# Kernel optimization log

Measured on AMD Instinct MI355X. Metric: run time of the kernel, lower is better.

Reference implementation:

```python
import jax, jax.numpy as jnp
import numpy as np

EPS = 1e-5

def _bn(x):
    # training-mode batchnorm (batch stats), gamma=1 beta=0 per the module's init
    ax = tuple(range(x.ndim - 1))
    m = x.mean(ax, keepdims=True)
    v = x.var(ax, keepdims=True)
    return (x - m) * jax.lax.rsqrt(v + EPS)

def _mlp(x, weights):
    # shared 1x1-conv MLP: pointwise linear -> BN -> ReLU
    for W in weights:
        x = jax.nn.relu(_bn(jnp.einsum('...c,oc->...o', x, W)))
    return x

def _fps_single(xyz, npoint):
    # farthest point sampling, xyz [N,3] -> [npoint] int32 indices
    N = xyz.shape[0]
    def step(carry, _):
        dists, far = carry
        d = jnp.sum((xyz - xyz[far]) ** 2, -1)
        dists = jnp.minimum(dists, d)
        return (dists, jnp.argmax(dists).astype(jnp.int32)), far
    init = (jnp.full((N,), 1e10, xyz.dtype), jnp.int32(0))
    _, idx = jax.lax.scan(step, init, None, length=npoint)
    return idx

def _ball_query(new_xyz, xyz, radius, nsample):
    # first nsample points (in original order) within radius of each center
    d2 = jnp.sum((new_xyz[:, :, None, :] - xyz[:, None, :, :]) ** 2, -1)  # [B,S,N]
    N = xyz.shape[1]
    rank = jnp.where(d2 < radius * radius, jnp.arange(N, dtype=jnp.int32), jnp.int32(N))
    vals, _ = jax.lax.top_k(-rank, nsample)
    idx = -vals
    idx = jnp.where(idx == N, idx[..., :1], idx)  # pad with first valid (center itself)
    return idx

def _gather(pts, idx):
    # pts [B,N,C], idx [B,S,ns] -> [B,S,ns,C]
    B, S, ns = idx.shape
    return jnp.take_along_axis(pts, idx.reshape(B, S * ns, 1), axis=1).reshape(B, S, ns, pts.shape[-1])

def _sa(xyz, feats, npoint, radius, nsample, weights):
    fps_idx = jax.vmap(_fps_single, in_axes=(0, None))(xyz, npoint)
    new_xyz = jnp.take_along_axis(xyz, fps_idx[:, :, None], axis=1)  # [B,S,3]
    idx = _ball_query(new_xyz, xyz, radius, nsample)
    g_xyz = (_gather(xyz, idx) - new_xyz[:, :, None, :]) / radius  # normalize_xyz
    x = g_xyz if feats is None else jnp.concatenate([g_xyz, _gather(feats, idx)], -1)
    x = _mlp(x, weights)
    return new_xyz, x.max(axis=2), fps_idx  # maxpool over nsample

def _forward(obj_cloud, gripper_cloud, sa1_w0, sa1_w1, sa1_w2, sa2_w0, sa2_w1, sa2_w2,
             sa3_w0, sa3_w1, sa3_w2, ge_w0, ge_w1, ge_w2,
             head_w0, head_b0, head_w1, head_b1, head_w2, head_b2):
    # gripper encoder: pointwise conv1d MLP + global maxpool
    g = _mlp(gripper_cloud, [ge_w0, ge_w1, ge_w2])      # [B,G,128]
    gripper_feature = g.max(axis=1)                      # [B,128]
    # backbone
    xyz1, f1, _ = _sa(obj_cloud, None, 512, 0.2, 32, [sa1_w0, sa1_w1, sa1_w2])
    xyz2, f2, _ = _sa(xyz1, f1, 128, 0.4, 64, [sa2_w0, sa2_w1, sa2_w2])
    # sa3: group_all (use_xyz, no centering/normalization)
    x = jnp.concatenate([xyz2, f2], -1)[:, None]         # [B,1,128,259]
    x = _mlp(x, [sa3_w0, sa3_w1, sa3_w2])
    obj_feature = x.max(axis=2)[:, 0]                    # [B,1024]
    comb = jnp.concatenate([gripper_feature, obj_feature], -1)  # [B,1152]
    h = _bn(comb)
    h = jax.nn.relu(_bn(h @ head_w0.T + head_b0))
    h = jax.nn.relu(_bn(h @ head_w1.T + head_b1))
    return jax.nn.relu(h @ head_w2.T + head_b2)          # [B,1]

def setup_inputs() -> dict:
    key = jax.random.key(0)
    ks = jax.random.split(key, 24)
    def w(k, o, i):
        return (jax.random.normal(k, (o, i), jnp.float32) * 0.05)
    inp = {
        'obj_cloud': jax.random.uniform(ks[0], (8, 20000, 3), jnp.float32),
        'gripper_cloud': jax.random.uniform(ks[1], (8, 512, 3), jnp.float32),
        'sa1_w0': w(ks[2], 64, 3),   'sa1_w1': w(ks[3], 64, 64),   'sa1_w2': w(ks[4], 128, 64),
        'sa2_w0': w(ks[5], 128, 131),'sa2_w1': w(ks[6], 128, 128), 'sa2_w2': w(ks[7], 256, 128),
        'sa3_w0': w(ks[8], 256, 259),'sa3_w1': w(ks[9], 512, 256), 'sa3_w2': w(ks[10], 1024, 512),
        'ge_w0': w(ks[11], 64, 3),   'ge_w1': w(ks[12], 128, 64),  'ge_w2': w(ks[13], 128, 128),
        'head_w0': w(ks[14], 512, 1152), 'head_b0': jnp.zeros((512,), jnp.float32),
        'head_w1': w(ks[15], 256, 512),  'head_b1': jnp.zeros((256,), jnp.float32),
        'head_w2': w(ks[16], 1, 256),    'head_b2': jnp.zeros((1,), jnp.float32),
    }
    return inp

def reference(obj_cloud, gripper_cloud, sa1_w0, sa1_w1, sa1_w2, sa2_w0, sa2_w1, sa2_w2,
              sa3_w0, sa3_w1, sa3_w2, ge_w0, ge_w1, ge_w2,
              head_w0, head_b0, head_w1, head_b1, head_w2, head_b2):
    return _forward(obj_cloud, gripper_cloud, sa1_w0, sa1_w1, sa1_w2, sa2_w0, sa2_w1, sa2_w2,
                    sa3_w0, sa3_w1, sa3_w2, ge_w0, ge_w1, ge_w2,
                    head_w0, head_b0, head_w1, head_b1, head_w2, head_b2)
```

## Files before the change

### kernel.cpp

```cpp
#include <hip/hip_runtime.h>
#include <cstddef>
#include <cstdint>

#define EPS_BN 1e-5f
#define NBINS 4
#define NEG_INF (-__builtin_inff())

template <bool FUSE_IN>
__global__ __launch_bounds__(256) void gemm_xwt(const float* __restrict__ X,
                                                const float* __restrict__ Wm,
                                                float* __restrict__ Y,
                                                int R, int Cin, int Cout,
                                                const float* __restrict__ st_in, int Rin,
                                                float* __restrict__ st_out) {
  __shared__ __align__(16) float Xs[16][132];
  __shared__ __align__(16) float Ws[16][132];
  __shared__ float sMean[512], sScale[512];
  const int t  = threadIdx.x;
  const int r0 = blockIdx.x << 7;
  const int n0 = blockIdx.y << 7;
  const int tx = t & 15;
  const int ty = t >> 4;

  if constexpr (FUSE_IN) {
    const float inv = 1.f / (float)Rin;
    for (int k = t; k < Cin; k += 256) {
      float s = 0.f, q = 0.f;
#pragma unroll
      for (int bn = 0; bn < NBINS; ++bn) {
        s += st_in[bn * 2 * Cin + k];
        q += st_in[bn * 2 * Cin + Cin + k];
      }
      const float m  = s * inv;
      const float vr = fmaf(-m, m, q * inv);
      sMean[k]  = m;
      sScale[k] = rsqrtf(vr + EPS_BN);
    }
    __syncthreads();
  }

  float acc[8][8] = {};
  const int rStage = t >> 1;
  const int kBase  = (t & 1) << 3;
  const int nr     = n0 + rStage;

  for (int k0 = 0; k0 < Cin; k0 += 16) {
    const float* xrow = X  + (size_t)(r0 + rStage) * Cin + k0 + kBase;
    const float* wrow = Wm + (size_t)nr * Cin + k0 + kBase;
    if (((Cin & 3) == 0) && (k0 + 16 <= Cin)) {
      float4 xa = *(const float4*)(xrow);
      float4 xb = *(const float4*)(xrow + 4);
      if constexpr (FUSE_IN) {
        const int kb = k0 + kBase;
        xa.x = fmaxf(0.f, (xa.x - sMean[kb + 0]) * sScale[kb + 0]);
        xa.y = fmaxf(0.f, (xa.y - sMean[kb + 1]) * sScale[kb + 1]);
        xa.z = fmaxf(0.f, (xa.z - sMean[kb + 2]) * sScale[kb + 2]);
        xa.w = fmaxf(0.f, (xa.w - sMean[kb + 3]) * sScale[kb + 3]);
        xb.x = fmaxf(0.f, (xb.x - sMean[kb + 4]) * sScale[kb + 4]);
        xb.y = fmaxf(0.f, (xb.y - sMean[kb + 5]) * sScale[kb + 5]);
        xb.z = fmaxf(0.f, (xb.z - sMean[kb + 6]) * sScale[kb + 6]);
        xb.w = fmaxf(0.f, (xb.w - sMean[kb + 7]) * sScale[kb + 7]);
      }
      Xs[kBase + 0][rStage] = xa.x; Xs[kBase + 1][rStage] = xa.y;
      Xs[kBase + 2][rStage] = xa.z; Xs[kBase + 3][rStage] = xa.w;
      Xs[kBase + 4][rStage] = xb.x; Xs[kBase + 5][rStage] = xb.y;
      Xs[kBase + 6][rStage] = xb.z; Xs[kBase + 7][rStage] = xb.w;
      float4 wa = {0, 0, 0, 0}, wb = {0, 0, 0, 0};
      if (nr < Cout) { wa = *(const float4*)(wrow); wb = *(const float4*)(wrow + 4); }
      Ws[kBase + 0][rStage] = wa.x; Ws[kBase + 1][rStage] = wa.y;
      Ws[kBase + 2][rStage] = wa.z; Ws[kBase + 3][rStage] = wa.w;
      Ws[kBase + 4][rStage] = wb.x; Ws[kBase + 5][rStage] = wb.y;
      Ws[kBase + 6][rStage] = wb.z; Ws[kBase + 7][rStage] = wb.w;
    } else {
#pragma unroll
      for (int u = 0; u < 8; ++u) {
        const int k = k0 + kBase + u;
        float xe = 0.f, we = 0.f;
        if (k < Cin) {
          xe = xrow[u];
          if constexpr (FUSE_IN) xe = fmaxf(0.f, (xe - sMean[k]) * sScale[k]);
          if (nr < Cout) we = wrow[u];
        }
        Xs[kBase + u][rStage] = xe;
        Ws[kBase + u][rStage] = we;
      }
    }
    __syncthreads();
#pragma unroll
    for (int kk = 0; kk < 16; ++kk) {
      const float4 a0 = *(const float4*)(&Xs[kk][ty << 2]);
      const float4 a1 = *(const float4*)(&Xs[kk][64 + (ty << 2)]);
      const float4 b0 = *(const float4*)(&Ws[kk][tx << 2]);
      const float4 b1 = *(const float4*)(&Ws[kk][64 + (tx << 2)]);
      const float av[8] = {a0.x, a0.y, a0.z, a0.w, a1.x, a1.y, a1.z, a1.w};
      const float bw[8] = {b0.x, b0.y, b0.z, b0.w, b1.x, b1.y, b1.z, b1.w};
#pragma unroll
      for (int i = 0; i < 8; ++i)
#pragma unroll
        for (int j = 0; j < 8; ++j) acc[i][j] = fmaf(av[i], bw[j], acc[i][j]);
    }
    __syncthreads();
  }
#pragma unroll
  for (int h = 0; h < 2; ++h)
#pragma unroll
    for (int i = 0; i < 4; ++i) {
      const int r = r0 + h * 64 + (ty << 2) + i;
      float* yr = Y + (size_t)r * Cout;
#pragma unroll
      for (int g = 0; g < 2; ++g) {
        const int n = n0 + g * 64 + (tx << 2);
        if (n < Cout) {
          float4 o = {acc[h * 4 + i][g * 4 + 0], acc[h * 4 + i][g * 4 + 1],
                      acc[h * 4 + i][g * 4 + 2], acc[h * 4 + i][g * 4 + 3]};
          *(float4*)(yr + n) = o;
        }
      }
    }
#pragma unroll
  for (int g = 0; g < 2; ++g)
#pragma unroll
    for (int j = 0; j < 4; ++j) {
      float s = 0.f, q = 0.f;
#pragma unroll
      for (int rh = 0; rh < 8; ++rh) {
        const float v = acc[rh][g * 4 + j];
        s += v;
        q = fmaf(v, v, q);
      }
      Xs[ty][g * 64 + (tx << 2) + j] = s;
      Ws[ty][g * 64 + (tx << 2) + j] = q;
    }
  __syncthreads();
  if (t < 128) {
    const int n = n0 + t;
    if (n < Cout) {
      float s = 0.f, q = 0.f;
#pragma unroll
      for (int w = 0; w < 16; ++w) { s += Xs[w][t]; q += Ws[w][t]; }
      float* dst = st_out + (blockIdx.x & (NBINS - 1)) * 2 * Cout;
      atomicAdd(dst + n, s);
      atomicAdd(dst + Cout + n, q);
    }
  }
}

__global__ void bn_apply_relu_maxpool(const float* __restrict__ Y,
                                      const float* __restrict__ st,
                                      float* __restrict__ o, int G, int ns, int C) {
  const int i = blockIdx.x * 256 + threadIdx.x;
  if (i >= G * C) return;
  const int c = i % C;
  const int g = i / C;
  float s = 0.f, q = 0.f;
#pragma unroll
  for (int bn = 0; bn < NBINS; ++bn) {
    s += st[bn * 2 * C + c];
    q += st[bn * 2 * C + C + c];
  }
  const int R = G * ns;
  const float inv = 1.f / (float)R;
  const float m  = s * inv;
  const float vr = fmaf(-m, m, q * inv);
  const float sc = rsqrtf(vr + EPS_BN);
  const float* p = Y + (size_t)g * ns * C + c;
  float mx = NEG_INF;
  for (int k = 0; k < ns; ++k) mx = fmaxf(mx, p[(size_t)k * C]);
  o[i] = fmaxf(0.f, (mx - m) * sc);
}

#define REPA(X) X(0) X(1) X(2) X(3) X(4) X(5) X(6) X(7) X(8) X(9) X(10) X(11)
#define REPB(X) X(12) X(13) X(14) X(15) X(16) X(17) X(18) X(19)

__global__ __launch_bounds__(1024)
void fps_sa1_kernel(const float* __restrict__ xyz, float* __restrict__ new_xyz) {
  const int b    = blockIdx.x;
  const int tid  = threadIdx.x;
  const int lane = tid & 63;
  const int wave = tid >> 6;
  const float* p = xyz + (size_t)b * 20000 * 3;

  __shared__ float ddL[12 * 1024];
  __shared__ float sv[16], sx[16], sy[16], sz[16];
  __shared__ int   si[16];
  __shared__ float bc[3];

#define DECLR(k) float px##k, py##k, pz##k, dd##k;
  REPB(DECLR)
#undef DECLR

#define INITL(k) ddL[(k) * 1024 + tid] = 1e10f;
  REPA(INITL)
#undef INITL
#define INITR(k) {                                                          \
    const int i = tid + (k) * 1024;                                         \
    if (i < 20000) {                                                        \
      px##k = p[i * 3 + 0]; py##k = p[i * 3 + 1]; pz##k = p[i * 3 + 2];     \
      dd##k = 1e10f;                                                        \
    } else {                                                                \
      px##k = 0.f; py##k = 0.f; pz##k = 0.f;                                \
      dd##k = NEG_INF;                                                      \
    } }
  REPB(INITR)
#undef INITR

  float fx = p[0], fy = p[1], fz = p[2];
  if (tid == 0) {
    float* o = new_xyz + (size_t)b * 512 * 3;
    o[0] = fx; o[1] = fy; o[2] = fz;
  }
  __syncthreads();

  for (int s = 1; s < 512; ++s) {
    float bv = NEG_INF;
    int   bi = 0x7fffffff;
    float bx = 0.f, by = 0.f, bz = 0.f;
#define SCANS(k) {                                                          \
    const int i = tid + (k) * 1024;                                         \
    const float qx = p[i * 3 + 0], qy = p[i * 3 + 1], qz = p[i * 3 + 2];    \
    const float dx = qx - fx, dy = qy - fy, dz = qz - fz;                   \
    const float d  = __fadd_rn(__fadd_rn(__fmul_rn(dx, dx), __fmul_rn(dy, dy)), \
                               __fmul_rn(dz, dz));                          \
    const float nd = fminf(ddL[(k) * 1024 + tid], d);                       \
    ddL[(k) * 1024 + tid] = nd;                                             \
    if (nd > bv) { bv = nd; bi = i; bx = qx; by = qy; bz = qz; } }
    REPA(SCANS)
#undef SCANS
#define SCANR(k) {                                                          \
    const float dx = px##k - fx, dy = py##k - fy, dz = pz##k - fz;          \
    const float d  = __fadd_rn(__fadd_rn(__fmul_rn(dx, dx), __fmul_rn(dy, dy)), \
                               __fmul_rn(dz, dz));                          \
    const float nd = fminf(dd##k, d);                                       \
    dd##k = nd;                                                             \
    if (nd > bv) { bv = nd; bi = tid + (k) * 1024;                          \
                   bx = px##k; by = py##k; bz = pz##k; } }
    REPB(SCANR)
#undef SCANR
    float v  = bv;
    int   i0 = bi;
#pragma unroll
    for (int m = 1; m < 64; m <<= 1) {
      const float ov = __shfl_xor(v, m, 64);
      const int   oi = __shfl_xor(i0, m, 64);
      if (ov > v || (ov == v && oi < i0)) { v = ov; i0 = oi; }
    }
    if (i0 == bi) {
      sv[wave] = bv; si[wave] = bi; sx[wave] = bx; sy[wave] = by; sz[wave] = bz;
    }
    __syncthreads();
    if (tid < 64) {
      const float lv = (lane < 16) ? sv[lane] : NEG_INF;
      const int   li = (lane < 16) ? si[lane] : 0x7fffffff;
      float v2 = lv;
      int   i2 = li;
#pragma unroll
      for (int m = 1; m < 16; m <<= 1) {
        const float ov = __shfl_xor(v2, m, 64);
        const int   oi = __shfl_xor(i2, m, 64);
        if (ov > v2 || (ov == v2 && oi < i2)) { v2 = ov; i2 = oi; }
      }
      if (lane < 16 && li == i2) {
        const float wx = sx[lane], wy = sy[lane], wz = sz[lane];
        bc[0] = wx; bc[1] = wy; bc[2] = wz;
        float* o = new_xyz + ((size_t)b * 512 + s) * 3;
        o[0] = wx; o[1] = wy; o[2] = wz;
      }
    }
    __syncthreads();
    fx = bc[0]; fy = bc[1]; fz = bc[2];
  }
}

template <int N, int NP, int THREADS, int NPT>
__global__ __launch_bounds__(THREADS)
void fps2_kernel(const float* __restrict__ xyz, float* __restrict__ new_xyz) {
  constexpr int NW = THREADS / 64;
  const int b    = blockIdx.x;
  const int tid  = threadIdx.x;
  const int lane = tid & 63;
  const int wave = tid >> 6;
  const float* p = xyz + (size_t)b * N * 3;
  float px[NPT], py[NPT], pz[NPT], dd[NPT];
#pragma unroll
  for (int j = 0; j < NPT; ++j) {
    const int i = tid + j * THREADS;
    if (i < N) {
      px[j] = p[i * 3 + 0];
      py[j] = p[i * 3 + 1];
      pz[j] = p[i * 3 + 2];
      dd[j] = 1e10f;
    } else {
      px[j] = 0.f; py[j] = 0.f; pz[j] = 0.f;
      dd[j] = NEG_INF;
    }
  }
  __shared__ float sv[NW], sx[NW], sy[NW], sz[NW];
  __shared__ int   si[NW];
  __shared__ float bc[3];
  float fx = p[0], fy = p[1], fz = p[2];
  if (tid == 0) {
    float* o = new_xyz + (size_t)b * NP * 3;
    o[0] = fx; o[1] = fy; o[2] = fz;
  }
  for (int s = 1; s < NP; ++s) {
    float bv = NEG_INF;
    int   bi = 0x7fffffff;
    float bx = 0.f, by = 0.f, bz = 0.f;
#pragma unroll
    for (int j = 0; j < NPT; ++j) {
      const float dx = px[j] - fx;
      const float dy = py[j] - fy;
      const float dz = pz[j] - fz;
      const float d  = __fadd_rn(__fadd_rn(__fmul_rn(dx, dx), __fmul_rn(dy, dy)),
                                 __fmul_rn(dz, dz));
      const float nd = fminf(dd[j], d);
      dd[j] = nd;
      if (nd > bv) { bv = nd; bi = tid + j * THREADS; bx = px[j]; by = py[j]; bz = pz[j]; }
    }
    float v = bv;
    int   i0 = bi;
#pragma unroll
    for (int m = 1; m < 64; m <<= 1) {
      const float ov = __shfl_xor(v, m, 64);
      const int   oi = __shfl_xor(i0, m, 64);
      if (ov > v || (ov == v && oi < i0)) { v = ov; i0 = oi; }
    }
    if (i0 == bi) {
      sv[wave] = bv; si[wave] = bi; sx[wave] = bx; sy[wave] = by; sz[wave] = bz;
    }
    __syncthreads();
    if (tid < 64) {
      const float lv = (lane < NW) ? sv[lane] : NEG_INF;
      const int   li = (lane < NW) ? si[lane] : 0x7fffffff;
      float v2 = lv;
      int   i2 = li;
#pragma unroll
      for (int m = 1; m < NW; m <<= 1) {
        const float ov = __shfl_xor(v2, m, 64);
        const int   oi = __shfl_xor(i2, m, 64);
        if (ov > v2 || (ov == v2 && oi < i2)) { v2 = ov; i2 = oi; }
      }
      if (lane < NW && li == i2) {
        const float wx = sx[lane], wy = sy[lane], wz = sz[lane];
        bc[0] = wx; bc[1] = wy; bc[2] = wz;
        float* o = new_xyz + ((size_t)b * NP + s) * 3;
        o[0] = wx; o[1] = wy; o[2] = wz;
      }
    }
    __syncthreads();
    fx = bc[0]; fy = bc[1]; fz = bc[2];
  }
}

template <int N, int NS>
__global__ __launch_bounds__(256)
void ballquery_wave_kernel(const float* __restrict__ centers,
                           const float* __restrict__ pts,
                           int* __restrict__ idx, int BS, int S, float r2) {
  const int w    = (blockIdx.x * 256 + threadIdx.x) >> 6;
  const int lane = threadIdx.x & 63;
  if (w >= BS) return;
  const int b = w / S;
  const float cx = centers[w * 3 + 0];
  const float cy = centers[w * 3 + 1];
  const float cz = centers[w * 3 + 2];
  const float* p = pts + (size_t)b * N * 3;
  int* o = idx + (size_t)w * NS;
  int total = 0;
  int first = -1;
  for (int i0 = 0; i0 < N && total < NS; i0 += 64) {
    const int i = i0 + lane;
    bool pred = false;
    if (i < N) {
      const float dx = cx - p[i * 3 + 0];
      const float dy = cy - p[i * 3 + 1];
      const float dz = cz - p[i * 3 + 2];
      const float d2 = __fadd_rn(__fadd_rn(__fmul_rn(dx, dx), __fmul_rn(dy, dy)),
                                 __fmul_rn(dz, dz));
      pred = (d2 < r2);
    }
    const unsigned long long mask = __ballot(pred);
    if (mask) {
      const unsigned long long below = (lane == 0) ? 0ull : (mask << (64 - lane));
      const int before = __popcll(below);
      if (pred && (total + before) < NS) o[total + before] = i;
      if (first < 0) first = i0 + (__ffsll((long long)mask) - 1);
      total += __popcll(mask);
    }
  }
  if (lane >= total && lane < NS) o[lane] = first;
}

__global__ void group1_kernel(const float* __restrict__ xyz, const float* __restrict__ ctr,
                              const int* __restrict__ idx, float* __restrict__ X1) {
  const int t = blockIdx.x * 256 + threadIdx.x;
  if (t >= 8 * 512 * 32) return;
  const int g = t >> 5;
  const int b = g >> 9;
  const int i = idx[t];
  const float* p = xyz + ((size_t)b * 20000 + i) * 3;
  const float* c = ctr + (size_t)g * 3;
  X1[t * 3 + 0] = (p[0] - c[0]) / 0.2f;
  X1[t * 3 + 1] = (p[1] - c[1]) / 0.2f;
  X1[t * 3 + 2] = (p[2] - c[2]) / 0.2f;
}

__global__ void group2_kernel(const float* __restrict__ xyz1,
                              const float* __restrict__ xyz2,
                              const float* __restrict__ f1,
                              const int* __restrict__ idx2,
                              float* __restrict__ X2) {
  const int t = blockIdx.x * 256 + threadIdx.x;
  if (t >= 65536 * 131) return;
  const int r = t / 131;
  const int c = t - r * 131;
  const int g = r >> 6;
  const int b = g >> 7;
  const int i = idx2[r];
  float v;
  if (c < 3) {
    v = (xyz1[((size_t)b * 512 + i) * 3 + c] - xyz2[(size_t)g * 3 + c]) / 0.4f;
  } else {
    v = f1[((size_t)b * 512 + i) * 128 + (c - 3)];
  }
  X2[t] = v;
}

__global__ void build_x3_kernel(const float* __restrict__ xyz2, const float* __restrict__ f2,
                                float* __restrict__ X3) {
  const int t = blockIdx.x * 256 + threadIdx.x;
  if (t >= 1024 * 259) return;
  const int r = t / 259;
  const int c = t - r * 259;
  X3[t] = (c < 3) ? xyz2[r * 3 + c] : f2[(size_t)r * 256 + (c - 3)];
}

__global__ __launch_bounds__(512) void head_kernel(
    const float* __restrict__ gfeat, const float* __restrict__ objf,
    const float* __restrict__ w0, const float* __restrict__ b0,
    const float* __restrict__ w1, const float* __restrict__ b1,
    const float* __restrict__ w2, const float* __restrict__ b2,
    float* __restrict__ out) {
  __shared__ __align__(16) float comb[8 * 1152];
  __shared__ __align__(16) float h1[8 * 512];
  __shared__ __align__(16) float h2[8 * 256];
  const int tid = threadIdx.x;
  for (int i = tid; i < 8 * 1152; i += 512) {
    const int b = i / 1152, c = i - b * 1152;
    comb[i] = (c < 128) ? gfeat[b * 128 + c] : objf[b * 1024 + (c - 128)];
  }
  __syncthreads();
  for (int c = tid; c < 1152; c += 512) {
    float s = 0.f;
#pragma unroll
    for (int b = 0; b < 8; ++b) s += comb[b * 1152 + c];
    const float m = s * 0.125f;
    float v = 0.f;
#pragma unroll
    for (int b = 0; b < 8; ++b) { const float d = comb[b * 1152 + c] - m; v = fmaf(d, d, v); }
    const float sc = rsqrtf(v * 0.125f + EPS_BN);
#pragma unroll
    for (int b = 0; b < 8; ++b) comb[b * 1152 + c] = (comb[b * 1152 + c] - m) * sc;
  }
  __syncthreads();
  {
    float a[8];
#pragma unroll
    for (int b = 0; b < 8; ++b) a[b] = b0[tid];
    const float* wr = w0 + (size_t)tid * 1152;
    for (int ci = 0; ci < 1152; ci += 4) {
      const float4 wv = *(const float4*)(wr + ci);
#pragma unroll
      for (int b = 0; b < 8; ++b) {
        const float4 xv = *(const float4*)(&comb[b * 1152 + ci]);
        a[b] = fmaf(xv.x, wv.x, a[b]);
        a[b] = fmaf(xv.y, wv.y, a[b]);
        a[b] = fmaf(xv.z, wv.z, a[b]);
        a[b] = fmaf(xv.w, wv.w, a[b]);
      }
    }
    float s = 0.f;
#pragma unroll
    for (int b = 0; b < 8; ++b) s += a[b];
    const float m = s * 0.125f;
    float v = 0.f;
#pragma unroll
    for (int b = 0; b < 8; ++b) { const float d = a[b] - m; v = fmaf(d, d, v); }
    const float sc = rsqrtf(v * 0.125f + EPS_BN);
#pragma unroll
    for (int b = 0; b < 8; ++b) h1[b * 512 + tid] = fmaxf(0.f, (a[b] - m) * sc);
  }
  __syncthreads();
  if (tid < 256) {
    float a[8];
#pragma unroll
    for (int b = 0; b < 8; ++b) a[b] = b1[tid];
    const float* wr = w1 + (size_t)tid * 512;
    for (int ci = 0; ci < 512; ci += 4) {
      const float4 wv = *(const float4*)(wr + ci);
#pragma unroll
      for (int b = 0; b < 8; ++b) {
        const float4 xv = *(const float4*)(&h1[b * 512 + ci]);
        a[b] = fmaf(xv.x, wv.x, a[b]);
        a[b] = fmaf(xv.y, wv.y, a[b]);
        a[b] = fmaf(xv.z, wv.z, a[b]);
        a[b] = fmaf(xv.w, wv.w, a[b]);
      }
    }
    float s = 0.f;
#pragma unroll
    for (int b = 0; b < 8; ++b) s += a[b];
    const float m = s * 0.125f;
    float v = 0.f;
#pragma unroll
    for (int b = 0; b < 8; ++b) { const float d = a[b] - m; v = fmaf(d, d, v); }
    const float sc = rsqrtf(v * 0.125f + EPS_BN);
#pragma unroll
    for (int b = 0; b < 8; ++b) h2[b * 256 + tid] = fmaxf(0.f, (a[b] - m) * sc);
  }
  __syncthreads();
  if (tid < 8) {
    float s = b2[0];
    for (int ci = 0; ci < 256; ++ci) s = fmaf(h2[tid * 256 + ci], w2[ci], s);
    out[tid] = fmaxf(0.f, s);
  }
}

extern "C" void kernel_launch(void* const* d_in, const int* in_sizes, int n_in,
                              void* d_out, int out_size, void* d_ws, size_t ws_size,
                              hipStream_t stream) {
  (void)in_sizes; (void)n_in; (void)out_size; (void)ws_size;
  const float* obj  = (const float*)d_in[0];
  const float* grip = (const float*)d_in[1];
  const float* s1w0 = (const float*)d_in[2];
  const float* s1w1 = (const float*)d_in[3];
  const float* s1w2 = (const float*)d_in[4];
  const float* s2w0 = (const float*)d_in[5];
  const float* s2w1 = (const float*)d_in[6];
  const float* s2w2 = (const float*)d_in[7];
  const float* s3w0 = (const float*)d_in[8];
  const float* s3w1 = (const float*)d_in[9];
  const float* s3w2 = (const float*)d_in[10];
  const float* gw0  = (const float*)d_in[11];
  const float* gw1  = (const float*)d_in[12];
  const float* gw2  = (const float*)d_in[13];
  const float* hw0  = (const float*)d_in[14];
  const float* hb0  = (const float*)d_in[15];
  const float* hw1  = (const float*)d_in[16];
  const float* hb1  = (const float*)d_in[17];
  const float* hw2  = (const float*)d_in[18];
  const float* hb2  = (const float*)d_in[19];
  float* out = (float*)d_out;

  float* wsf   = (float*)d_ws;
  float* stats = wsf;
  float* xyz1  = wsf + 23040;
  float* xyz2  = wsf + 35328;
  float* gfeat = wsf + 38400;
  float* objf  = wsf + 39424;
  float* f1    = wsf + 47616;
  float* f2    = wsf + 571904;
  float* x3    = wsf + 834048;
  int*   idx1  = (int*)(wsf + 1099264);
  int*   idx2  = (int*)(wsf + 1230336);
  float* bufP  = wsf + 1295872;
  float* bufQ  = wsf + 18073088;

  static const int st_off[12] = {0, 512, 1536, 2560, 3072, 3584,
                                 4608, 5632, 6656, 8704, 10752, 14848};
  auto st = [&](int li) { return stats + st_off[li]; };

  hipMemsetAsync(stats, 0, 23040 * sizeof(float), stream);

  auto gemm0 = [&](const float* X, const float* Wm, float* Y, int R, int Cin, int Cout,
                   int lo) {
    dim3 g((R + 127) / 128, (Cout + 127) / 128);
    gemm_xwt<false><<<g, 256, 0, stream>>>(X, Wm, Y, R, Cin, Cout, nullptr, 0, st(lo));
  };
  auto gemmf = [&](const float* X, const float* Wm, float* Y, int R, int Cin, int Cout,
                   int li, int lo) {
    dim3 g((R + 127) / 128, (Cout + 127) / 128);
    gemm_xwt<true><<<g, 256, 0, stream>>>(X, Wm, Y, R, Cin, Cout, st(li), R, st(lo));
  };
  auto applymax_k = [&](const float* Y, int li, int G, int ns, int C, float* o) {
    const int n = G * C;
    bn_apply_relu_maxpool<<<(n + 255) / 256, 256, 0, stream>>>(Y, st(li), o, G, ns, C);
  };

  fps_sa1_kernel<<<8, 1024, 0, stream>>>(obj, xyz1);

  float* gY1 = bufP;
  float* gY2 = bufP + 262144;
  float* gY3 = bufP + 786432;
  gemm0(grip, gw0, gY1, 4096, 3, 64, 0);
  gemmf(gY1, gw1, gY2, 4096, 64, 128, 0, 1);
  gemmf(gY2, gw2, gY3, 4096, 128, 128, 1, 2);
  applymax_k(gY3, 2, 8, 512, 128, gfeat);

  ballquery_wave_kernel<20000, 32><<<1024, 256, 0, stream>>>(xyz1, obj, idx1, 4096, 512, 0.04f);
  float* X1 = bufQ;
  group1_kernel<<<512, 256, 0, stream>>>(obj, xyz1, idx1, X1);
  gemm0(X1, s1w0, bufP, 131072, 3, 64, 3);
  gemmf(bufP, s1w1, bufQ, 131072, 64, 64, 3, 4);
  gemmf(bufQ, s1w2, bufP, 131072, 64, 128, 4, 5);
  applymax_k(bufP, 5, 4096, 32, 128, f1);

  fps2_kernel<512, 128, 256, 2><<<8, 256, 0, stream>>>(xyz1, xyz2);
  ballquery_wave_kernel<512, 64><<<256, 256, 0, stream>>>(xyz2, xyz1, idx2, 1024, 128, 0.16f);
  float* X2 = bufQ;
  group2_kernel<<<(65536 * 131 + 255) / 256, 256, 0, stream>>>(xyz1, xyz2, f1, idx2, X2);
  gemm0(X2, s2w0, bufP, 65536, 131, 128, 6);
  gemmf(bufP, s2w1, bufQ, 65536, 128, 128, 6, 7);
  gemmf(bufQ, s2w2, bufP, 65536, 128, 256, 7, 8);
  applymax_k(bufP, 8, 1024, 64, 256, f2);

  build_x3_kernel<<<(1024 * 259 + 255) / 256, 256, 0, stream>>>(xyz2, f2, x3);
  float* Y3a = bufQ;
  float* Y3b = bufQ + 262144;
  float* Y3c = bufQ + 786432;
  gemm0(x3, s3w0, Y3a, 1024, 259, 256, 9);
  gemmf(Y3a, s3w1, Y3b, 1024, 256, 512, 9, 10);
  gemmf(Y3b, s3w2, Y3c, 1024, 512, 1024, 10, 11);
  applymax_k(Y3c, 11, 8, 128, 1024, objf);

  head_kernel<<<1, 512, 0, stream>>>(gfeat, objf, hw0, hb0, hw1, hb1, hw2, hb2, out);
}
```

Before: 2.489 ms.

## Sort FPS points by Morton cell and skip threads via bounding-box pruning

Adds a pre-pass that bins each cloud's 20000 points into a 16^3 Morton grid and writes them spatially sorted as float4 (xyz plus original index) into a scratch buffer. The FPS kernel then gives each thread 20 contiguous sorted points with a per-thread bounding box. When the new far point is farther from the box than the thread's current best distance, the thread skips its distance update entirely. This cuts the per-iteration distance work across 511 serial steps, at the cost of an extra sort kernel and a larger LDS distance array. Ties are broken by the original index so results stay identical.

Measured after the change: 3.016 ms. 21.2% more time.

```diff
diff --git a/kernel.cpp b/kernel.cpp
--- a/kernel.cpp
+++ b/kernel.cpp
@@ -169,40 +169,95 @@
   o[i] = fmaxf(0.f, (mx - m) * sc);
 }
 
-#define REPA(X) X(0) X(1) X(2) X(3) X(4) X(5) X(6) X(7) X(8) X(9) X(10) X(11)
-#define REPB(X) X(12) X(13) X(14) X(15) X(16) X(17) X(18) X(19)
+__device__ inline int fps_cell(float x, float y, float z) {
+  int cx = (int)(x * 16.f); cx = cx < 0 ? 0 : (cx > 15 ? 15 : cx);
+  int cy = (int)(y * 16.f); cy = cy < 0 ? 0 : (cy > 15 ? 15 : cy);
+  int cz = (int)(z * 16.f); cz = cz < 0 ? 0 : (cz > 15 ? 15 : cz);
+  auto sp = [](int v) { return (v & 1) | ((v & 2) << 2) | ((v & 4) << 4) | ((v & 8) << 6); };
+  return sp(cx) | (sp(cy) << 1) | (sp(cz) << 2);
+}
 
 __global__ __launch_bounds__(1024)
-void fps_sa1_kernel(const float* __restrict__ xyz, float* __restrict__ new_xyz) {
+void fps_sort_kernel(const float* __restrict__ xyz, float4* __restrict__ sorted) {
+  const int b = blockIdx.x, tid = threadIdx.x;
+  const float* p = xyz + (size_t)b * 20000 * 3;
+  __shared__ int hist[4096];
+  __shared__ int base[4096];
+  __shared__ int wsum[64];
+  for (int i = tid; i < 4096; i += 1024) hist[i] = 0;
+  __syncthreads();
+#pragma unroll
+  for (int k = 0; k < 20; ++k) {
+    const int i = tid + k * 1024;
+    if (i < 20000) atomicAdd(&hist[fps_cell(p[i * 3], p[i * 3 + 1], p[i * 3 + 2])], 1);
+  }
+  __syncthreads();
+  if (tid < 64) {
+    int s = 0;
+    for (int j = 0; j < 64; ++j) s += hist[tid * 64 + j];
+    wsum[tid] = s;
+  }
+  __syncthreads();
+  if (tid == 0) {
+    int r = 0;
+    for (int j = 0; j < 64; ++j) { const int v = wsum[j]; wsum[j] = r; r += v; }
+  }
+  __syncthreads();
+  if (tid < 64) {
+    int r = wsum[tid];
+    for (int j = 0; j < 64; ++j) { const int c = tid * 64 + j; const int h = hist[c]; base[c] = r; r += h; }
+  }
+  __syncthreads();
+  float4* sb = sorted + (size_t)b * 20480;
+#pragma unroll
+  for (int k = 0; k < 20; ++k) {
+    const int i = tid + k * 1024;
+    if (i < 20000) {
+      const float x = p[i * 3], y = p[i * 3 + 1], z = p[i * 3 + 2];
+      const int pos = atomicAdd(&base[fps_cell(x, y, z)], 1);
+      float4 q; q.x = x; q.y = y; q.z = z; q.w = __int_as_float(i);
+      sb[pos] = q;
+    }
+  }
+  const float x0 = p[0], y0 = p[1], z0 = p[2];
+  for (int i = 20000 + tid; i < 20480; i += 1024) {
+    float4 q; q.x = x0; q.y = y0; q.z = z0; q.w = __int_as_float(0x3fffffff);
+    sb[i] = q;
+  }
+}
+
+__global__ __launch_bounds__(1024)
+void fps_sa1_kernel(const float* __restrict__ xyz, const float4* __restrict__ sorted,
+                    float* __restrict__ new_xyz) {
   const int b    = blockIdx.x;
   const int tid  = threadIdx.x;
   const int lane = tid & 63;
   const int wave = tid >> 6;
   const float* p = xyz + (size_t)b * 20000 * 3;
-
-  __shared__ float ddL[12 * 1024];
+  const float4* sp = sorted + (size_t)b * 20480 + tid * 20;
+
+  __shared__ float ddL[20 * 1024];
   __shared__ float sv[16], sx[16], sy[16], sz[16];
   __shared__ int   si[16];
   __shared__ float bc[3];
 
-#define DECLR(k) float px##k, py##k, pz##k, dd##k;
-  REPB(DECLR)
-#undef DECLR
-
-#define INITL(k) ddL[(k) * 1024 + tid] = 1e10f;
-  REPA(INITL)
-#undef INITL
-#define INITR(k) {                                                          \
-    const int i = tid + (k) * 1024;                                         \
-    if (i < 20000) {                                                        \
-      px##k = p[i * 3 + 0]; py##k = p[i * 3 + 1]; pz##k = p[i * 3 + 2];     \
-      dd##k = 1e10f;                                                        \
-    } else {                                                                \
-      px##k = 0.f; py##k = 0.f; pz##k = 0.f;                                \
-      dd##k = NEG_INF;                                                      \
-    } }
-  REPB(INITR)
-#undef INITR
+  float mnx = 1e30f, mny = 1e30f, mnz = 1e30f;
+  float mxx = -1e30f, mxy = -1e30f, mxz = -1e30f;
+  float cbv = NEG_INF, cbx = 0.f, cby = 0.f, cbz = 0.f;
+  int   cbi = 0x7fffffff;
+
+#pragma unroll
+  for (int j = 0; j < 20; ++j) {
+    const float4 q = sp[j];
+    const int qi = __float_as_int(q.w);
+    mnx = fminf(mnx, q.x); mny = fminf(mny, q.y); mnz = fminf(mnz, q.z);
+    mxx = fmaxf(mxx, q.x); mxy = fmaxf(mxy, q.y); mxz = fmaxf(mxz, q.z);
+    const float d0 = (qi < 20000) ? 1e10f : NEG_INF;
+    ddL[j * 1024 + tid] = d0;
+    if (d0 > cbv || (d0 == cbv && qi < cbi)) {
+      cbv = d0; cbi = qi; cbx = q.x; cby = q.y; cbz = q.z;
+    }
+  }
 
   float fx = p[0], fy = p[1], fz = p[2];
   if (tid == 0) {
@@ -212,40 +267,38 @@
   __syncthreads();
 
   for (int s = 1; s < 512; ++s) {
-    float bv = NEG_INF;
-    int   bi = 0x7fffffff;
-    float bx = 0.f, by = 0.f, bz = 0.f;
-#define SCANS(k) {                                                          \
-    const int i = tid + (k) * 1024;                                         \
-    const float qx = p[i * 3 + 0], qy = p[i * 3 + 1], qz = p[i * 3 + 2];    \
-    const float dx = qx - fx, dy = qy - fy, dz = qz - fz;                   \
-    const float d  = __fadd_rn(__fadd_rn(__fmul_rn(dx, dx), __fmul_rn(dy, dy)), \
-                               __fmul_rn(dz, dz));                          \
-    const float nd = fminf(ddL[(k) * 1024 + tid], d);                       \
-    ddL[(k) * 1024 + tid] = nd;                                             \
-    if (nd > bv) { bv = nd; bi = i; bx = qx; by = qy; bz = qz; } }
-    REPA(SCANS)
-#undef SCANS
-#define SCANR(k) {                                                          \
-    const float dx = px##k - fx, dy = py##k - fy, dz = pz##k - fz;          \
-    const float d  = __fadd_rn(__fadd_rn(__fmul_rn(dx, dx), __fmul_rn(dy, dy)), \
-                               __fmul_rn(dz, dz));                          \
-    const float nd = fminf(dd##k, d);                                       \
-    dd##k = nd;                                                             \
-    if (nd > bv) { bv = nd; bi = tid + (k) * 1024;                          \
-                   bx = px##k; by = py##k; bz = pz##k; } }
-    REPB(SCANR)
-#undef SCANR
-    float v  = bv;
-    int   i0 = bi;
+    const float ax = fmaxf(fmaxf(mnx - fx, fx - mxx), 0.f);
+    const float ay = fmaxf(fmaxf(mny - fy, fy - mxy), 0.f);
+    const float az = fmaxf(fmaxf(mnz - fz, fz - mxz), 0.f);
+    const float dm = __fadd_rn(__fadd_rn(__fmul_rn(ax, ax), __fmul_rn(ay, ay)),
+                               __fmul_rn(az, az));
+    if (dm < cbv) {
+      cbv = NEG_INF; cbi = 0x7fffffff;
+#pragma unroll
+      for (int j = 0; j < 20; ++j) {
+        const float4 q = sp[j];
+        const int qi = __float_as_int(q.w);
+        const float dx = q.x - fx, dy = q.y - fy, dz = q.z - fz;
+        const float d = __fadd_rn(__fadd_rn(__fmul_rn(dx, dx), __fmul_rn(dy, dy)),
+                                  __fmul_rn(dz, dz));
+        const int a = j * 1024 + tid;
+        const float nd = fminf(ddL[a], d);
+        ddL[a] = nd;
+        if (nd > cbv || (nd == cbv && qi < cbi)) {
+          cbv = nd; cbi = qi; cbx = q.x; cby = q.y; cbz = q.z;
+        }
+      }
+    }
+    float v  = cbv;
+    int   i0 = cbi;
 #pragma unroll
     for (int m = 1; m < 64; m <<= 1) {
       const float ov = __shfl_xor(v, m, 64);
       const int   oi = __shfl_xor(i0, m, 64);
       if (ov > v || (ov == v && oi < i0)) { v = ov; i0 = oi; }
     }
-    if (i0 == bi) {
-      sv[wave] = bv; si[wave] = bi; sx[wave] = bx; sy[wave] = by; sz[wave] = bz;
+    if (i0 == cbi) {
+      sv[wave] = cbv; si[wave] = cbi; sx[wave] = cbx; sy[wave] = cby; sz[wave] = cbz;
     }
     __syncthreads();
     if (tid < 64) {
@@ -587,7 +640,9 @@
     bn_apply_relu_maxpool<<<(n + 255) / 256, 256, 0, stream>>>(Y, st(li), o, G, ns, C);
   };
 
-  fps_sa1_kernel<<<8, 1024, 0, stream>>>(obj, xyz1);
+  float4* sorted = (float4*)bufP;
+  fps_sort_kernel<<<8, 1024, 0, stream>>>(obj, sorted);
+  fps_sa1_kernel<<<8, 1024, 0, stream>>>(obj, sorted, xyz1);
 
   float* gY1 = bufP;
   float* gY2 = bufP + 262144;
```

## Restructure SA1 FPS: contiguous per-thread points, float4 loads, single-barrier reduction

Applied to the files above, without the earlier changes.

Each thread in the SA1 farthest-point-sampling kernel now owns 20 contiguous points instead of strided ones. The 12 spilled points are read with float4 vector loads, and threads at or above 1000 are padded with -inf distances. The cross-wave argmax reduction now uses double-buffered shared slots that every thread scans redundantly, which drops one __syncthreads and the single-wave shuffle stage per iteration. The trade-off is more LDS reads per thread and uneven thread utilisation (24 idle threads).

After: 2.769 ms. 11.3% more time.

```diff
diff --git a/kernel.cpp b/kernel.cpp
--- a/kernel.cpp
+++ b/kernel.cpp
@@ -169,39 +169,32 @@
   o[i] = fmaxf(0.f, (mx - m) * sc);
 }
 
-#define REPA(X) X(0) X(1) X(2) X(3) X(4) X(5) X(6) X(7) X(8) X(9) X(10) X(11)
-#define REPB(X) X(12) X(13) X(14) X(15) X(16) X(17) X(18) X(19)
+#define REPB7(X) X(12) X(13) X(14) X(15) X(16) X(17) X(18) X(19)
 
 __global__ __launch_bounds__(1024)
 void fps_sa1_kernel(const float* __restrict__ xyz, float* __restrict__ new_xyz) {
   const int b    = blockIdx.x;
   const int tid  = threadIdx.x;
-  const int lane = tid & 63;
   const int wave = tid >> 6;
   const float* p = xyz + (size_t)b * 20000 * 3;
+  const bool real = (tid < 1000);
+  const int  base = real ? tid * 20 : 0;
+  const float4* sp4 = (const float4*)(p + (size_t)base * 3);
 
   __shared__ float ddL[12 * 1024];
-  __shared__ float sv[16], sx[16], sy[16], sz[16];
-  __shared__ int   si[16];
-  __shared__ float bc[3];
+  __shared__ __align__(8) float2 sVI[2][16];
+  __shared__ float sxw[2][16], syw[2][16], szw[2][16];
 
 #define DECLR(k) float px##k, py##k, pz##k, dd##k;
-  REPB(DECLR)
+  REPB7(DECLR)
 #undef DECLR
 
-#define INITL(k) ddL[(k) * 1024 + tid] = 1e10f;
-  REPA(INITL)
-#undef INITL
+  for (int j = 0; j < 12; ++j) ddL[j * 1024 + tid] = real ? 1e10f : NEG_INF;
 #define INITR(k) {                                                          \
-    const int i = tid + (k) * 1024;                                         \
-    if (i < 20000) {                                                        \
-      px##k = p[i * 3 + 0]; py##k = p[i * 3 + 1]; pz##k = p[i * 3 + 2];     \
-      dd##k = 1e10f;                                                        \
-    } else {                                                                \
-      px##k = 0.f; py##k = 0.f; pz##k = 0.f;                                \
-      dd##k = NEG_INF;                                                      \
-    } }
-  REPB(INITR)
+    const int i = base + (k);                                               \
+    px##k = p[i * 3 + 0]; py##k = p[i * 3 + 1]; pz##k = p[i * 3 + 2];       \
+    dd##k = real ? 1e10f : NEG_INF; }
+  REPB7(INITR)
 #undef INITR
 
   float fx = p[0], fy = p[1], fz = p[2];
@@ -212,29 +205,39 @@
   __syncthreads();
 
   for (int s = 1; s < 512; ++s) {
+    const int par = s & 1;
     float bv = NEG_INF;
     int   bi = 0x7fffffff;
     float bx = 0.f, by = 0.f, bz = 0.f;
-#define SCANS(k) {                                                          \
-    const int i = tid + (k) * 1024;                                         \
-    const float qx = p[i * 3 + 0], qy = p[i * 3 + 1], qz = p[i * 3 + 2];    \
-    const float dx = qx - fx, dy = qy - fy, dz = qz - fz;                   \
-    const float d  = __fadd_rn(__fadd_rn(__fmul_rn(dx, dx), __fmul_rn(dy, dy)), \
-                               __fmul_rn(dz, dz));                          \
-    const float nd = fminf(ddL[(k) * 1024 + tid], d);                       \
-    ddL[(k) * 1024 + tid] = nd;                                             \
-    if (nd > bv) { bv = nd; bi = i; bx = qx; by = qy; bz = qz; } }
-    REPA(SCANS)
-#undef SCANS
+#pragma unroll
+    for (int g = 0; g < 3; ++g) {
+      const float4 qa = sp4[g * 3 + 0];
+      const float4 qb = sp4[g * 3 + 1];
+      const float4 qc = sp4[g * 3 + 2];
+#define PROC(jj, QX, QY, QZ) {                                              \
+      const int j = g * 4 + (jj);                                           \
+      const float dx = (QX) - fx, dy = (QY) - fy, dz = (QZ) - fz;           \
+      const float d = __fadd_rn(__fadd_rn(__fmul_rn(dx, dx), __fmul_rn(dy, dy)), \
+                                __fmul_rn(dz, dz));                         \
+      const int a = j * 1024 + tid;                                         \
+      const float nd = fminf(ddL[a], d);                                    \
+      ddL[a] = nd;                                                          \
+      if (nd > bv) { bv = nd; bi = base + j; bx = (QX); by = (QY); bz = (QZ); } }
+      PROC(0, qa.x, qa.y, qa.z)
+      PROC(1, qa.w, qb.x, qb.y)
+      PROC(2, qb.z, qb.w, qc.x)
+      PROC(3, qc.y, qc.z, qc.w)
+#undef PROC
+    }
 #define SCANR(k) {                                                          \
     const float dx = px##k - fx, dy = py##k - fy, dz = pz##k - fz;          \
     const float d  = __fadd_rn(__fadd_rn(__fmul_rn(dx, dx), __fmul_rn(dy, dy)), \
                                __fmul_rn(dz, dz));                          \
     const float nd = fminf(dd##k, d);                                       \
     dd##k = nd;                                                             \
-    if (nd > bv) { bv = nd; bi = tid + (k) * 1024;                          \
+    if (nd > bv) { bv = nd; bi = base + (k);                                \
                    bx = px##k; by = py##k; bz = pz##k; } }
-    REPB(SCANR)
+    REPB7(SCANR)
 #undef SCANR
     float v  = bv;
     int   i0 = bi;
@@ -245,29 +248,28 @@
       if (ov > v || (ov == v && oi < i0)) { v = ov; i0 = oi; }
     }
     if (i0 == bi) {
-      sv[wave] = bv; si[wave] = bi; sx[wave] = bx; sy[wave] = by; sz[wave] = bz;
+      float2 e; e.x = bv; e.y = __int_as_float(bi);
+      sVI[par][wave] = e;
+      sxw[par][wave] = bx; syw[par][wave] = by; szw[par][wave] = bz;
     }
     __syncthreads();
-    if (tid < 64) {
-      const float lv = (lane < 16) ? sv[lane] : NEG_INF;
-      const int   li = (lane < 16) ? si[lane] : 0x7fffffff;
-      float v2 = lv;
-      int   i2 = li;
-#pragma unroll
-      for (int m = 1; m < 16; m <<= 1) {
-        const float ov = __shfl_xor(v2, m, 64);
-        const int   oi = __shfl_xor(i2, m, 64);
-        if (ov > v2 || (ov == v2 && oi < i2)) { v2 = ov; i2 = oi; }
-      }
-      if (lane < 16 && li == i2) {
-        const float wx = sx[lane], wy = sy[lane], wz = sz[lane];
-        bc[0] = wx; bc[1] = wy; bc[2] = wz;
-        float* o = new_xyz + ((size_t)b * 512 + s) * 3;
-        o[0] = wx; o[1] = wy; o[2] = wz;
-      }
-    }
-    __syncthreads();
-    fx = bc[0]; fy = bc[1]; fz = bc[2];
+    int ww = 0;
+    {
+      float2 e = sVI[par][0];
+      float wv = e.x;
+      int   wi = __float_as_int(e.y);
+#pragma unroll
+      for (int w = 1; w < 16; ++w) {
+        e = sVI[par][w];
+        const int ei = __float_as_int(e.y);
+        if (e.x > wv || (e.x == wv && ei < wi)) { wv = e.x; wi = ei; ww = w; }
+      }
+    }
+    fx = sxw[par][ww]; fy = syw[par][ww]; fz = szw[par][ww];
+    if (tid == 0) {
+      float* o = new_xyz + ((size_t)b * 512 + s) * 3;
+      o[0] = fx; o[1] = fy; o[2] = fz;
+    }
   }
 }
 
```

## Fuse max-pool into final MLP GEMM epilogue, apply BN after pooling

Applied to the files above, without the earlier changes.

The last GEMM of each set-abstraction MLP no longer writes its full pre-activation output. It reduces the max over each neighbourhood group inside the tile epilogue and writes only pooled values. A small kernel then applies batch-norm and ReLU to the pooled result, which relies on BN-ReLU being monotone increasing with unit gamma. This removes large global writes and reads of the intermediate activations, at the cost of extra shared-memory passes and syncs in the epilogue.

After: 2.412 ms. 3.1% less time.

```diff
diff --git a/kernel.cpp b/kernel.cpp
--- a/kernel.cpp
+++ b/kernel.cpp
@@ -6,13 +6,14 @@
 #define NBINS 4
 #define NEG_INF (-__builtin_inff())
 
-template <bool FUSE_IN>
+template <bool FUSE_IN, bool FUSE_MAX>
 __global__ __launch_bounds__(256) void gemm_xwt(const float* __restrict__ X,
                                                 const float* __restrict__ Wm,
                                                 float* __restrict__ Y,
                                                 int R, int Cin, int Cout,
                                                 const float* __restrict__ st_in, int Rin,
-                                                float* __restrict__ st_out) {
+                                                float* __restrict__ st_out,
+                                                float* __restrict__ pooled, int ns) {
   __shared__ __align__(16) float Xs[16][132];
   __shared__ __align__(16) float Ws[16][132];
   __shared__ float sMean[512], sScale[512];
@@ -101,22 +102,24 @@
     }
     __syncthreads();
   }
-#pragma unroll
-  for (int h = 0; h < 2; ++h)
-#pragma unroll
-    for (int i = 0; i < 4; ++i) {
-      const int r = r0 + h * 64 + (ty << 2) + i;
-      float* yr = Y + (size_t)r * Cout;
-#pragma unroll
-      for (int g = 0; g < 2; ++g) {
-        const int n = n0 + g * 64 + (tx << 2);
-        if (n < Cout) {
-          float4 o = {acc[h * 4 + i][g * 4 + 0], acc[h * 4 + i][g * 4 + 1],
-                      acc[h * 4 + i][g * 4 + 2], acc[h * 4 + i][g * 4 + 3]};
-          *(float4*)(yr + n) = o;
+  if constexpr (!FUSE_MAX) {
+#pragma unroll
+    for (int h = 0; h < 2; ++h)
+#pragma unroll
+      for (int i = 0; i < 4; ++i) {
+        const int r = r0 + h * 64 + (ty << 2) + i;
+        float* yr = Y + (size_t)r * Cout;
+#pragma unroll
+        for (int g = 0; g < 2; ++g) {
+          const int n = n0 + g * 64 + (tx << 2);
+          if (n < Cout) {
+            float4 o = {acc[h * 4 + i][g * 4 + 0], acc[h * 4 + i][g * 4 + 1],
+                        acc[h * 4 + i][g * 4 + 2], acc[h * 4 + i][g * 4 + 3]};
+            *(float4*)(yr + n) = o;
+          }
         }
       }
-    }
+  }
 #pragma unroll
   for (int g = 0; g < 2; ++g)
 #pragma unroll
@@ -143,6 +146,66 @@
       atomicAdd(dst + Cout + n, q);
     }
   }
+  if constexpr (FUSE_MAX) {
+    __syncthreads();
+    float mxAll = NEG_INF;
+#pragma unroll
+    for (int h = 0; h < 2; ++h) {
+#pragma unroll
+      for (int g2 = 0; g2 < 2; ++g2)
+#pragma unroll
+        for (int j = 0; j < 4; ++j) {
+          float mx = acc[h * 4 + 0][g2 * 4 + j];
+          mx = fmaxf(mx, acc[h * 4 + 1][g2 * 4 + j]);
+          mx = fmaxf(mx, acc[h * 4 + 2][g2 * 4 + j]);
+          mx = fmaxf(mx, acc[h * 4 + 3][g2 * 4 + j]);
+          Xs[ty][g2 * 64 + (tx << 2) + j] = mx;
+        }
+      __syncthreads();
+      if (t < 128) {
+        const int n = n0 + t;
+        if (n < Cout) {
+          if (ns <= 64) {
+            const int tpg = ns >> 2;
+            const int gph = 64 / ns;
+            for (int gq = 0; gq < gph; ++gq) {
+              float mx = NEG_INF;
+              for (int w = gq * tpg; w < gq * tpg + tpg; ++w) mx = fmaxf(mx, Xs[w][t]);
+              const int g = (r0 + h * 64) / ns + gq;
+              pooled[(size_t)g * Cout + n] = mx;
+            }
+          } else {
+            float mx = NEG_INF;
+            for (int w = 0; w < 16; ++w) mx = fmaxf(mx, Xs[w][t]);
+            mxAll = fmaxf(mxAll, mx);
+          }
+        }
+      }
+      __syncthreads();
+    }
+    if (ns > 64 && t < 128) {
+      const int n = n0 + t;
+      if (n < Cout) pooled[(size_t)(r0 >> 7) * Cout + n] = mxAll;
+    }
+  }
+}
+
+__global__ void bn_apply_pooled(const float* __restrict__ P, const float* __restrict__ st,
+                                float* __restrict__ o, int G, int C, int Rtrue) {
+  const int i = blockIdx.x * 256 + threadIdx.x;
+  if (i >= G * C) return;
+  const int c = i % C;
+  float s = 0.f, q = 0.f;
+#pragma unroll
+  for (int bn = 0; bn < NBINS; ++bn) {
+    s += st[bn * 2 * C + c];
+    q += st[bn * 2 * C + C + c];
+  }
+  const float inv = 1.f / (float)Rtrue;
+  const float m  = s * inv;
+  const float vr = fmaf(-m, m, q * inv);
+  const float sc = rsqrtf(vr + EPS_BN);
+  o[i] = fmaxf(0.f, (P[i] - m) * sc);
 }
 
 __global__ void bn_apply_relu_maxpool(const float* __restrict__ Y,
@@ -575,16 +638,28 @@
   auto gemm0 = [&](const float* X, const float* Wm, float* Y, int R, int Cin, int Cout,
                    int lo) {
     dim3 g((R + 127) / 128, (Cout + 127) / 128);
-    gemm_xwt<false><<<g, 256, 0, stream>>>(X, Wm, Y, R, Cin, Cout, nullptr, 0, st(lo));
+    gemm_xwt<false, false><<<g, 256, 0, stream>>>(X, Wm, Y, R, Cin, Cout, nullptr, 0,
+                                                  st(lo), nullptr, 0);
   };
   auto gemmf = [&](const float* X, const float* Wm, float* Y, int R, int Cin, int Cout,
                    int li, int lo) {
     dim3 g((R + 127) / 128, (Cout + 127) / 128);
-    gemm_xwt<true><<<g, 256, 0, stream>>>(X, Wm, Y, R, Cin, Cout, st(li), R, st(lo));
+    gemm_xwt<true, false><<<g, 256, 0, stream>>>(X, Wm, Y, R, Cin, Cout, st(li), R,
+                                                 st(lo), nullptr, 0);
+  };
+  auto gemmfM = [&](const float* X, const float* Wm, float* pooled, int R, int Cin,
+                    int Cout, int li, int lo, int ns) {
+    dim3 g((R + 127) / 128, (Cout + 127) / 128);
+    gemm_xwt<true, true><<<g, 256, 0, stream>>>(X, Wm, nullptr, R, Cin, Cout, st(li), R,
+                                                st(lo), pooled, ns);
   };
   auto applymax_k = [&](const float* Y, int li, int G, int ns, int C, float* o) {
     const int n = G * C;
     bn_apply_relu_maxpool<<<(n + 255) / 256, 256, 0, stream>>>(Y, st(li), o, G, ns, C);
+  };
+  auto applypool_k = [&](const float* P, int li, int G, int C, int Rtrue, float* o) {
+    const int n = G * C;
+    bn_apply_pooled<<<(n + 255) / 256, 256, 0, stream>>>(P, st(li), o, G, C, Rtrue);
   };
 
   fps_sa1_kernel<<<8, 1024, 0, stream>>>(obj, xyz1);
@@ -602,8 +677,8 @@
   group1_kernel<<<512, 256, 0, stream>>>(obj, xyz1, idx1, X1);
   gemm0(X1, s1w0, bufP, 131072, 3, 64, 3);
   gemmf(bufP, s1w1, bufQ, 131072, 64, 64, 3, 4);
-  gemmf(bufQ, s1w2, bufP, 131072, 64, 128, 4, 5);
-  applymax_k(bufP, 5, 4096, 32, 128, f1);
+  gemmfM(bufQ, s1w2, bufP, 131072, 64, 128, 4, 5, 32);
+  applypool_k(bufP, 5, 4096, 128, 131072, f1);
 
   fps2_kernel<512, 128, 256, 2><<<8, 256, 0, stream>>>(xyz1, xyz2);
   ballquery_wave_kernel<512, 64><<<256, 256, 0, stream>>>(xyz2, xyz1, idx2, 1024, 128, 0.16f);
@@ -611,17 +686,17 @@
   group2_kernel<<<(65536 * 131 + 255) / 256, 256, 0, stream>>>(xyz1, xyz2, f1, idx2, X2);
   gemm0(X2, s2w0, bufP, 65536, 131, 128, 6);
   gemmf(bufP, s2w1, bufQ, 65536, 128, 128, 6, 7);
-  gemmf(bufQ, s2w2, bufP, 65536, 128, 256, 7, 8);
-  applymax_k(bufP, 8, 1024, 64, 256, f2);
+  gemmfM(bufQ, s2w2, bufP, 65536, 128, 256, 7, 8, 64);
+  applypool_k(bufP, 8, 1024, 256, 65536, f2);
 
   build_x3_kernel<<<(1024 * 259 + 255) / 256, 256, 0, stream>>>(xyz2, f2, x3);
   float* Y3a = bufQ;
   float* Y3b = bufQ + 262144;
-  float* Y3c = bufQ + 786432;
+  float* Y3p = bufQ + 786432;
   gemm0(x3, s3w0, Y3a, 1024, 259, 256, 9);
   gemmf(Y3a, s3w1, Y3b, 1024, 256, 512, 9, 10);
-  gemmf(Y3b, s3w2, Y3c, 1024, 512, 1024, 10, 11);
-  applymax_k(Y3c, 11, 8, 128, 1024, objf);
+  gemmfM(Y3b, s3w2, Y3p, 1024, 512, 1024, 10, 11, 128);
+  applypool_k(Y3p, 11, 8, 1024, 1024, objf);
 
   head_kernel<<<1, 512, 0, stream>>>(gfeat, objf, hw0, hb0, hw1, hb1, hw2, hb2, out);
 }
```
